# Kernel tuning notes

Measured on AMD Instinct MI355X. Metric: run time of the kernel, lower is better.

The kernel has to match this reference:

```python
import jax, jax.numpy as jnp
import numpy as np
import math

B, S, D, H = 2, 2048, 2048, 16
HD = D // H            # 128
FF = 4 * D             # 8192
EPS = 1e-5


def _alibi_slopes(num_heads):
    # power-of-2 path (16 heads): slopes = base^i, base = 2^(-2^-(log2(n)-3))
    closest = 2 ** math.floor(math.log2(num_heads))
    base = 2.0 ** (-(2.0 ** (-(math.log2(closest) - 3))))
    powers = np.arange(1, 1 + closest, dtype=np.float32)
    slopes = base ** powers
    if closest != num_heads:
        extra_base = 2.0 ** (-(2.0 ** (-(math.log2(2 * closest) - 3))))
        num_rem = min(closest, num_heads - closest)
        extra_powers = np.arange(1, 1 + 2 * num_rem, 2, dtype=np.float32)
        slopes = np.concatenate([slopes, extra_base ** extra_powers])
    return jnp.asarray(slopes, dtype=jnp.float32)


def setup_inputs() -> dict:
    key = jax.random.key(0)
    ks = jax.random.split(key, 8)
    s = 0.02
    return {
        "x": jax.random.normal(ks[0], (B, S, D), dtype=jnp.float32),
        "ln1_w": jnp.ones((D,), jnp.float32),
        "ln1_b": jnp.zeros((D,), jnp.float32),
        "wqkv": jax.random.normal(ks[1], (D, 3 * D), jnp.float32) * s,
        "bqkv": jnp.zeros((3 * D,), jnp.float32),
        "wo": jax.random.normal(ks[2], (D, D), jnp.float32) * s,
        "bo": jnp.zeros((D,), jnp.float32),
        "ln2_w": jnp.ones((D,), jnp.float32),
        "ln2_b": jnp.zeros((D,), jnp.float32),
        "w1": jax.random.normal(ks[3], (D, FF), jnp.float32) * s,
        "b1": jnp.zeros((FF,), jnp.float32),
        "w2": jax.random.normal(ks[4], (FF, D), jnp.float32) * s,
        "b2": jnp.zeros((D,), jnp.float32),
    }


def _ln(x, w, b):
    mu = jnp.mean(x, axis=-1, keepdims=True)
    var = jnp.mean(jnp.square(x - mu), axis=-1, keepdims=True)
    return (x - mu) * jax.lax.rsqrt(var + EPS) * w + b


def reference(x, ln1_w, ln1_b, wqkv, bqkv, wo, bo, ln2_w, ln2_b, w1, b1, w2, b2):
    slopes = _alibi_slopes(H)                      # [H]
    # --- input layernorm + attention ---
    h = _ln(x, ln1_w, ln1_b)
    qkv = h @ wqkv + bqkv                          # [B,S,3D]
    q, k, v = jnp.split(qkv, 3, axis=-1)
    q = q.reshape(B, S, H, HD).transpose(0, 2, 1, 3)  # [B,H,S,HD]
    k = k.reshape(B, S, H, HD).transpose(0, 2, 1, 3)
    v = v.reshape(B, S, H, HD).transpose(0, 2, 1, 3)
    scores = jnp.einsum("bhqd,bhkd->bhqk", q, k) / math.sqrt(HD)
    pos = jnp.arange(S, dtype=jnp.float32)
    rel = pos[None, :] - pos[:, None]              # j - i
    alibi = slopes[:, None, None] * rel[None]      # [H,S,S]
    scores = scores.astype(jnp.float32) + alibi[None]
    causal = rel <= 0                              # j <= i
    scores = jnp.where(causal[None, None], scores, jnp.finfo(jnp.float32).min)
    probs = jax.nn.softmax(scores, axis=-1).astype(x.dtype)
    attn = jnp.einsum("bhqk,bhkd->bhqd", probs, v)  # [B,H,S,HD]
    attn = attn.transpose(0, 2, 1, 3).reshape(B, S, D)
    x = x + attn @ wo + bo
    # --- post-attn layernorm + GELU MLP ---
    h2 = _ln(x, ln2_w, ln2_b)
    m = jax.nn.gelu(h2 @ w1 + b1, approximate=True) @ w2 + b2
    return x + m
```

## Files before the change

### kernel.cpp

```cpp
#include <hip/hip_runtime.h>
#include <hip/hip_bf16.h>
#include <stdint.h>

#define BB 2
#define SS 2048
#define DD 2048
#define HH 16
#define HD 128
#define FFD 8192
#define TD (3*DD)

typedef unsigned short u16;
typedef __attribute__((ext_vector_type(8))) short s16x8;
typedef __attribute__((ext_vector_type(4))) float f32x4;

struct alignas(8) U16x4 { u16 a, b, c, d; };

__device__ __forceinline__ u16 f2b(float f) {
  union { float f; uint32_t u; } v; v.f = f;
  uint32_t r = (v.u + 0x7fffu + ((v.u >> 16) & 1u)) >> 16;
  return (u16)r;
}

__device__ __forceinline__ void async16(const void* g, void* l) {
  __builtin_amdgcn_global_load_lds((const __attribute__((address_space(1))) void*)g,
                                   (__attribute__((address_space(3))) void*)l,
                                   16, 0, 0);
}

__global__ __launch_bounds__(256) void wconv_t(const float* __restrict__ W,
                                               u16* __restrict__ Wt, int K, int N) {
  __shared__ float tile[64][65];
  int k0 = blockIdx.x * 64, n0 = blockIdx.y * 64;
  int c = threadIdx.x & 63, r0 = threadIdx.x >> 6;
#pragma unroll
  for (int i = 0; i < 16; ++i) {
    int r = i * 4 + r0;
    tile[r][c] = W[(size_t)(k0 + r) * N + n0 + c];
  }
  __syncthreads();
#pragma unroll
  for (int i = 0; i < 16; ++i) {
    int n = i * 4 + r0;
    Wt[(size_t)(n0 + n) * K + k0 + c] = f2b(tile[c][n]);
  }
}

__global__ __launch_bounds__(256) void ln_kernel(const float* __restrict__ X,
                                                 const float* __restrict__ g,
                                                 const float* __restrict__ be,
                                                 u16* __restrict__ O) {
  int row = blockIdx.x;
  const float* xr = X + (size_t)row * DD;
  int t = threadIdx.x;
  float4 v0 = ((const float4*)xr)[t];
  float4 v1 = ((const float4*)xr)[t + 256];
  float s = v0.x + v0.y + v0.z + v0.w + v1.x + v1.y + v1.z + v1.w;
  float q = v0.x*v0.x + v0.y*v0.y + v0.z*v0.z + v0.w*v0.w
          + v1.x*v1.x + v1.y*v1.y + v1.z*v1.z + v1.w*v1.w;
#pragma unroll
  for (int o = 32; o > 0; o >>= 1) { s += __shfl_down(s, o); q += __shfl_down(q, o); }
  __shared__ float red[8];
  if ((t & 63) == 0) { red[t >> 6] = s; red[4 + (t >> 6)] = q; }
  __syncthreads();
  float S = red[0] + red[1] + red[2] + red[3];
  float Q = red[4] + red[5] + red[6] + red[7];
  float mu = S * (1.0f / DD);
  float var = Q * (1.0f / DD) - mu * mu;
  float rs = rsqrtf(var + 1e-5f);
  float4 g0 = ((const float4*)g)[t],  g1 = ((const float4*)g)[t + 256];
  float4 b0 = ((const float4*)be)[t], b1 = ((const float4*)be)[t + 256];
  U16x4 o0, o1;
  o0.a = f2b((v0.x - mu) * rs * g0.x + b0.x);
  o0.b = f2b((v0.y - mu) * rs * g0.y + b0.y);
  o0.c = f2b((v0.z - mu) * rs * g0.z + b0.z);
  o0.d = f2b((v0.w - mu) * rs * g0.w + b0.w);
  o1.a = f2b((v1.x - mu) * rs * g1.x + b1.x);
  o1.b = f2b((v1.y - mu) * rs * g1.y + b1.y);
  o1.c = f2b((v1.z - mu) * rs * g1.z + b1.z);
  o1.d = f2b((v1.w - mu) * rs * g1.w + b1.w);
  *(U16x4*)(O + (size_t)row * DD + t * 4)         = o0;
  *(U16x4*)(O + (size_t)row * DD + (t + 256) * 4) = o1;
}

template <int MODE>
__global__ __launch_bounds__(512, 2) void gemm8(const u16* __restrict__ A,
                                                const u16* __restrict__ Bt,
                                                const float* __restrict__ bias,
                                                const float* __restrict__ res,
                                                void* __restrict__ Cout,
                                                int M, int N, int K) {
  __shared__ __align__(16) u16 As[2][2][256 * 32];
  __shared__ __align__(16) u16 Bs[2][2][128 * 32];

  int n0 = blockIdx.x * 128, m0 = blockIdx.y * 256;
  int tid = threadIdx.x;
  int lane = tid & 63, w = tid >> 6;
  int wn = w & 1, wm = w >> 1;
  int col = lane & 15, quad = lane >> 4;

  int r = tid >> 2, sl = tid & 3;
  int gks = (sl ^ ((r >> 1) & 3)) * 8;
  const u16* ag = A  + (size_t)(m0 + r) * K + gks;
  const u16* bg = Bt + (size_t)(n0 + r) * K + gks;

  int swz = (col >> 1) & 3;
  int aoff = (wm * 64) * 32 + col * 32 + ((quad ^ swz) * 8);
  int boff = (wn * 64) * 32 + col * 32 + ((quad ^ swz) * 8);

  f32x4 acc[4][4] = {};
  int ntiles = K >> 6;

#pragma unroll
  for (int kh = 0; kh < 2; ++kh) {
    async16(ag + kh * 32, &As[0][kh][tid * 8]);
    async16(ag + (size_t)128 * K + kh * 32, &As[0][kh][4096 + tid * 8]);
    async16(bg + kh * 32, &Bs[0][kh][tid * 8]);
  }
  asm volatile("s_waitcnt vmcnt(0)" ::: "memory");
  __builtin_amdgcn_s_barrier();

  for (int t = 0; t < ntiles; ++t) {
    int p = t & 1, pn = p ^ 1;
    const u16* agn = ag + (t + 1) * 64;
    const u16* bgn = bg + (t + 1) * 64;
    bool pf = (t + 1 < ntiles);
#pragma unroll
    for (int kh = 0; kh < 2; ++kh) {
      const u16* as_ = As[p][kh];
      const u16* bs_ = Bs[p][kh];
      s16x8 af[4], bf[4];
#pragma unroll
      for (int i = 0; i < 4; ++i)
        bf[i] = *(const s16x8*)&bs_[boff + i * 512];
#pragma unroll
      for (int i = 0; i < 4; ++i)
        af[i] = *(const s16x8*)&as_[aoff + i * 512];
      if (pf) {
        async16(agn + kh * 32, &As[pn][kh][tid * 8]);
        async16(agn + (size_t)128 * K + kh * 32, &As[pn][kh][4096 + tid * 8]);
        async16(bgn + kh * 32, &Bs[pn][kh][tid * 8]);
        asm volatile("s_waitcnt vmcnt(3)" ::: "memory");
      } else if (kh == 0) {
        asm volatile("s_waitcnt vmcnt(0)" ::: "memory");
      }
      __builtin_amdgcn_s_barrier();
      __builtin_amdgcn_s_setprio(1);
#pragma unroll
      for (int i = 0; i < 4; ++i)
#pragma unroll
        for (int j = 0; j < 4; ++j)
          acc[i][j] = __builtin_amdgcn_mfma_f32_16x16x32_bf16(
              af[i], bf[j], acc[i][j], 0, 0, 0);
      __builtin_amdgcn_s_setprio(0);
      __builtin_amdgcn_s_barrier();
    }
  }

#pragma unroll
  for (int mt = 0; mt < 4; ++mt) {
    int mg = m0 + wm * 64 + mt * 16 + quad * 4;
#pragma unroll
    for (int nt = 0; nt < 4; ++nt) {
      int ng = n0 + wn * 64 + nt * 16 + col;
      float bn = bias[ng];
#pragma unroll
      for (int rr = 0; rr < 4; ++rr) {
        float v = acc[mt][nt][rr] + bn;
        size_t idx = (size_t)(mg + rr) * N + ng;
        if (MODE == 1) {
          float u = 1.5957691216057308f * (v + 0.044715f * v * v * v);
          v = v / (1.0f + __expf(-u));
        }
        if (MODE == 2) {
          ((float*)Cout)[idx] = v + res[idx];
        } else {
          ((u16*)Cout)[idx] = f2b(v);
        }
      }
    }
  }
}

__global__ __launch_bounds__(256) void attn_kernel(const u16* __restrict__ qkv,
                                                   u16* __restrict__ out) {
  __shared__ __align__(16) u16 Ks[2][64 * 128];
  __shared__ __align__(16) u16 Vts[128 * 64];
  __shared__ __align__(16) u16 Ps[4][16 * 72];
  int bx = blockIdx.x, h = blockIdx.y, b = blockIdx.z;
  int tid = threadIdx.x, lane = tid & 63, w = tid >> 6;
  int col = lane & 15, quad = lane >> 4;
  const u16* base  = qkv + (size_t)b * SS * TD + (size_t)h * HD;
  const u16* kbase = base + DD;
  const u16* vbase = base + 2 * DD;
  float slope = exp2f(-0.5f * (float)(h + 1));
  const float scale = 0.088388347648318447f;
  int krow = tid >> 4;
  int ghb = (tid & 15) ^ (krow & 7);
  int vkey_loc = tid >> 4;
  int vhd0 = (tid & 15) * 8;
  int kxc = 8 * (tid & 7);

#pragma unroll 1
  for (int ph = 0; ph < 2; ++ph) {
    int qt = ph ? (31 - bx) : bx;
    int q0 = qt * 64;
    int ntile = qt + 1;
    int qr = q0 + w * 16 + col;
    s16x8 qf[4];
#pragma unroll
    for (int c = 0; c < 4; ++c)
      qf[c] = *(const s16x8*)(base + (size_t)qr * TD + c * 32 + quad * 8);
    float m_i[4] = {-1e30f, -1e30f, -1e30f, -1e30f};
    float l_i[4] = {0.f, 0.f, 0.f, 0.f};
    f32x4 oacc[8] = {};
#pragma unroll
    for (int s = 0; s < 4; ++s)
      async16(kbase + (size_t)(s * 16 + krow) * TD + ghb * 8,
              &Ks[0][s * 2048 + tid * 8]);
    s16x8 vreg[4];
#pragma unroll
    for (int s = 0; s < 4; ++s)
      vreg[s] = *(const s16x8*)(vbase + (size_t)(s * 16 + vkey_loc) * TD + vhd0);

    for (int t = 0; t < ntile; ++t) {
      int j0 = t * 64;
      __syncthreads();
      if (t + 1 < ntile) {
#pragma unroll
        for (int s = 0; s < 4; ++s)
          async16(kbase + (size_t)(j0 + 64 + s * 16 + krow) * TD + ghb * 8,
                  &Ks[(t + 1) & 1][s * 2048 + tid * 8]);
      }
#pragma unroll
      for (int s = 0; s < 4; ++s) {
        int key = s * 16 + vkey_loc;
#pragma unroll
        for (int j = 0; j < 8; ++j)
          Vts[(vhd0 + j) * 64 + (key ^ kxc)] = (u16)vreg[s][j];
      }
      if (t + 1 < ntile) {
#pragma unroll
        for (int s = 0; s < 4; ++s)
          vreg[s] = *(const s16x8*)(vbase + (size_t)(j0 + 64 + s * 16 + vkey_loc) * TD + vhd0);
      }
      const u16* kt_ = Ks[t & 1];
      f32x4 sc[4];
#pragma unroll
      for (int nt = 0; nt < 4; ++nt) {
        f32x4 s4 = {0.f, 0.f, 0.f, 0.f};
        int key = nt * 16 + col;
        int ksw = col & 7;
#pragma unroll
        for (int c = 0; c < 4; ++c) {
          s16x8 kf = *(const s16x8*)&kt_[key * 128 + (((c * 4 + quad) ^ ksw) * 8)];
          s4 = __builtin_amdgcn_mfma_f32_16x16x32_bf16(qf[c], kf, s4, 0, 0, 0);
        }
        sc[nt] = s4;
      }
      int rb = q0 + w * 16 + quad * 4;
      float p[4][4];
      float mt_[4] = {-1e30f, -1e30f, -1e30f, -1e30f};
#pragma unroll
      for (int nt = 0; nt < 4; ++nt) {
        int j = j0 + nt * 16 + col;
#pragma unroll
        for (int rr = 0; rr < 4; ++rr) {
          float v = sc[nt][rr] * scale + slope * (float)(j - (rb + rr));
          if (j > rb + rr) v = -1e30f;
          p[nt][rr] = v;
          mt_[rr] = fmaxf(mt_[rr], v);
        }
      }
#pragma unroll
      for (int o = 1; o < 16; o <<= 1)
#pragma unroll
        for (int rr = 0; rr < 4; ++rr) mt_[rr] = fmaxf(mt_[rr], __shfl_xor(mt_[rr], o));
      float alpha[4];
#pragma unroll
      for (int rr = 0; rr < 4; ++rr) {
        float mn = fmaxf(m_i[rr], mt_[rr]);
        alpha[rr] = __expf(m_i[rr] - mn);
        m_i[rr] = mn;
      }
      float ls[4] = {0.f, 0.f, 0.f, 0.f};
#pragma unroll
      for (int nt = 0; nt < 4; ++nt)
#pragma unroll
        for (int rr = 0; rr < 4; ++rr) {
          float e = __expf(p[nt][rr] - m_i[rr]);
          p[nt][rr] = e;
          ls[rr] += e;
        }
#pragma unroll
      for (int o = 1; o < 16; o <<= 1)
#pragma unroll
        for (int rr = 0; rr < 4; ++rr) ls[rr] += __shfl_xor(ls[rr], o);
#pragma unroll
      for (int rr = 0; rr < 4; ++rr) l_i[rr] = l_i[rr] * alpha[rr] + ls[rr];
#pragma unroll
      for (int ot = 0; ot < 8; ++ot)
#pragma unroll
        for (int rr = 0; rr < 4; ++rr) oacc[ot][rr] *= alpha[rr];
#pragma unroll
      for (int nt = 0; nt < 4; ++nt)
#pragma unroll
        for (int rr = 0; rr < 4; ++rr)
          Ps[w][(quad * 4 + rr) * 72 + nt * 16 + col] = f2b(p[nt][rr]);
      __syncthreads();
#pragma unroll
      for (int kt = 0; kt < 2; ++kt) {
        s16x8 pf = *(const s16x8*)&Ps[w][col * 72 + kt * 32 + quad * 8];
        int k8 = kt * 32 + quad * 8;
#pragma unroll
        for (int ot = 0; ot < 8; ++ot) {
          int hd = ot * 16 + col;
          int swz = 8 * ((hd >> 3) & 7);
          s16x8 vf = *(const s16x8*)&Vts[hd * 64 + (k8 ^ swz)];
          oacc[ot] = __builtin_amdgcn_mfma_f32_16x16x32_bf16(pf, vf, oacc[ot], 0, 0, 0);
        }
      }
    }
#pragma unroll
    for (int rr = 0; rr < 4; ++rr) l_i[rr] = 1.0f / l_i[rr];
    u16* ob = out + ((size_t)b * SS + q0 + w * 16 + quad * 4) * DD + h * HD;
#pragma unroll
    for (int ot = 0; ot < 8; ++ot)
#pragma unroll
      for (int rr = 0; rr < 4; ++rr)
        ob[(size_t)rr * DD + ot * 16 + col] = f2b(oacc[ot][rr] * l_i[rr]);
  }
}

extern "C" void kernel_launch(void* const* d_in, const int* in_sizes, int n_in,
                              void* d_out, int out_size, void* d_ws, size_t ws_size,
                              hipStream_t stream) {
  const float* x    = (const float*)d_in[0];
  const float* ln1w = (const float*)d_in[1];
  const float* ln1b = (const float*)d_in[2];
  const float* wqkv = (const float*)d_in[3];
  const float* bqkv = (const float*)d_in[4];
  const float* wo   = (const float*)d_in[5];
  const float* bo   = (const float*)d_in[6];
  const float* ln2w = (const float*)d_in[7];
  const float* ln2b = (const float*)d_in[8];
  const float* w1   = (const float*)d_in[9];
  const float* b1   = (const float*)d_in[10];
  const float* w2   = (const float*)d_in[11];
  const float* b2   = (const float*)d_in[12];

  const int M = BB * SS;
  char* ws = (char*)d_ws;
  u16*  wt   = (u16*)ws;
  u16*  qkv  = (u16*)(ws + 33554432ull);
  u16*  cbuf = (u16*)(ws + 33554432ull + 50331648ull);
  float* r1  = (float*)(ws + 33554432ull + 50331648ull + 67108864ull);
  u16* h1 = cbuf;
  u16* attn = cbuf;
  u16* m1 = cbuf;
  u16* h2 = qkv;

  ln_kernel<<<M, 256, 0, stream>>>(x, ln1w, ln1b, h1);
  wconv_t<<<dim3(DD / 64, TD / 64), 256, 0, stream>>>(wqkv, wt, DD, TD);
  gemm8<0><<<dim3(TD / 128, M / 256), 512, 0, stream>>>(h1, wt, bqkv, nullptr, qkv, M, TD, DD);
  attn_kernel<<<dim3(16, HH, BB), 256, 0, stream>>>(qkv, attn);
  wconv_t<<<dim3(DD / 64, DD / 64), 256, 0, stream>>>(wo, wt, DD, DD);
  gemm8<2><<<dim3(DD / 128, M / 256), 512, 0, stream>>>(attn, wt, bo, x, r1, M, DD, DD);
  ln_kernel<<<M, 256, 0, stream>>>(r1, ln2w, ln2b, h2);
  wconv_t<<<dim3(DD / 64, FFD / 64), 256, 0, stream>>>(w1, wt, DD, FFD);
  gemm8<1><<<dim3(FFD / 128, M / 256), 512, 0, stream>>>(h2, wt, b1, nullptr, m1, M, FFD, DD);
  wconv_t<<<dim3(FFD / 64, DD / 64), 256, 0, stream>>>(w2, wt, FFD, DD);
  gemm8<2><<<dim3(DD / 128, M / 256), 512, 0, stream>>>(m1, wt, b2, r1, (float*)d_out, M, DD, FFD);
}
```

Measured before the change: 912.5 us.

## Add 256x256-tile bf16 GEMM kernel for QKV and FFN-up projections

Adds a new GEMM kernel with 256x256 output tiles, a 64-wide K step split into two 32-wide LDS halves, double-buffered async global-to-LDS loads interleaved with MFMA work, and raised wave priority around the MFMA blocks. It replaces the 256x128 tile kernel for the QKV and W1 projections, the two widest-N GEMMs. The aim is to raise arithmetic intensity and cut global and LDS traffic per FLOP. The grids become smaller: 24x16 blocks for QKV and 32x16 for W1. The kernel uses 128 KB of LDS and 128 accumulator floats per thread, which can limit occupancy and wave fill.

```diff
diff --git a/kernel.cpp b/kernel.cpp
--- a/kernel.cpp
+++ b/kernel.cpp
@@ -182,6 +182,114 @@
   }
 }
 
+template <int MODE>
+__global__ __launch_bounds__(512, 2) void gemm256(const u16* __restrict__ A,
+                                                  const u16* __restrict__ Bt,
+                                                  const float* __restrict__ bias,
+                                                  const float* __restrict__ res,
+                                                  void* __restrict__ Cout,
+                                                  int M, int N, int K) {
+  __shared__ __align__(16) u16 As[2][2][256 * 32];
+  __shared__ __align__(16) u16 Bs[2][2][256 * 32];
+
+  int n0 = blockIdx.x * 256, m0 = blockIdx.y * 256;
+  int tid = threadIdx.x;
+  int lane = tid & 63, w = tid >> 6;
+  int wn = w & 3, wm = w >> 2;
+  int col = lane & 15, quad = lane >> 4;
+
+  int r = tid >> 2, sl = tid & 3;
+  int gks = (sl ^ ((r >> 1) & 3)) * 8;
+  const u16* ag = A  + (size_t)(m0 + r) * K + gks;
+  const u16* bg = Bt + (size_t)(n0 + r) * K + gks;
+
+  int swz = (col >> 1) & 3;
+  int aoff = (wm * 128 + col) * 32 + ((quad ^ swz) * 8);
+  int boff = (wn * 64 + col) * 32 + ((quad ^ swz) * 8);
+
+  f32x4 acc[8][4] = {};
+  int ntiles = K >> 6;
+
+#pragma unroll
+  for (int kh = 0; kh < 2; ++kh) {
+    async16(ag + kh * 32, &As[0][kh][tid * 8]);
+    async16(ag + (size_t)128 * K + kh * 32, &As[0][kh][4096 + tid * 8]);
+    async16(bg + kh * 32, &Bs[0][kh][tid * 8]);
+    async16(bg + (size_t)128 * K + kh * 32, &Bs[0][kh][4096 + tid * 8]);
+  }
+  asm volatile("s_waitcnt vmcnt(0)" ::: "memory");
+  __builtin_amdgcn_s_barrier();
+
+  for (int t = 0; t < ntiles; ++t) {
+    int p = t & 1, pn = p ^ 1;
+    const u16* agn = ag + (t + 1) * 64;
+    const u16* bgn = bg + (t + 1) * 64;
+    bool pf = (t + 1 < ntiles);
+#pragma unroll
+    for (int kh = 0; kh < 2; ++kh) {
+      const u16* as_ = As[p][kh];
+      const u16* bs_ = Bs[p][kh];
+      s16x8 bf[4];
+#pragma unroll
+      for (int j = 0; j < 4; ++j)
+        bf[j] = *(const s16x8*)&bs_[boff + j * 512];
+#pragma unroll
+      for (int q = 0; q < 2; ++q) {
+        s16x8 af[4];
+#pragma unroll
+        for (int i = 0; i < 4; ++i)
+          af[i] = *(const s16x8*)&as_[aoff + q * 2048 + i * 512];
+        if (pf) {
+          if (q == 0) {
+            async16(agn + kh * 32, &As[pn][kh][tid * 8]);
+            async16(agn + (size_t)128 * K + kh * 32, &As[pn][kh][4096 + tid * 8]);
+          } else {
+            async16(bgn + kh * 32, &Bs[pn][kh][tid * 8]);
+            async16(bgn + (size_t)128 * K + kh * 32, &Bs[pn][kh][4096 + tid * 8]);
+            asm volatile("s_waitcnt vmcnt(4)" ::: "memory");
+          }
+        } else if (kh == 0 && q == 1) {
+          asm volatile("s_waitcnt vmcnt(0)" ::: "memory");
+        }
+        __builtin_amdgcn_s_barrier();
+        __builtin_amdgcn_s_setprio(1);
+#pragma unroll
+        for (int i = 0; i < 4; ++i)
+#pragma unroll
+          for (int j = 0; j < 4; ++j)
+            acc[q * 4 + i][j] = __builtin_amdgcn_mfma_f32_16x16x32_bf16(
+                af[i], bf[j], acc[q * 4 + i][j], 0, 0, 0);
+        __builtin_amdgcn_s_setprio(0);
+        __builtin_amdgcn_s_barrier();
+      }
+    }
+  }
+
+#pragma unroll
+  for (int mt = 0; mt < 8; ++mt) {
+    int mg = m0 + wm * 128 + mt * 16 + quad * 4;
+#pragma unroll
+    for (int nt = 0; nt < 4; ++nt) {
+      int ng = n0 + wn * 64 + nt * 16 + col;
+      float bn = bias[ng];
+#pragma unroll
+      for (int rr = 0; rr < 4; ++rr) {
+        float v = acc[mt][nt][rr] + bn;
+        size_t idx = (size_t)(mg + rr) * N + ng;
+        if (MODE == 1) {
+          float u = 1.5957691216057308f * (v + 0.044715f * v * v * v);
+          v = v / (1.0f + __expf(-u));
+        }
+        if (MODE == 2) {
+          ((float*)Cout)[idx] = v + res[idx];
+        } else {
+          ((u16*)Cout)[idx] = f2b(v);
+        }
+      }
+    }
+  }
+}
+
 __global__ __launch_bounds__(256) void attn_kernel(const u16* __restrict__ qkv,
                                                    u16* __restrict__ out) {
   __shared__ __align__(16) u16 Ks[2][64 * 128];
@@ -362,13 +470,13 @@
 
   ln_kernel<<<M, 256, 0, stream>>>(x, ln1w, ln1b, h1);
   wconv_t<<<dim3(DD / 64, TD / 64), 256, 0, stream>>>(wqkv, wt, DD, TD);
-  gemm8<0><<<dim3(TD / 128, M / 256), 512, 0, stream>>>(h1, wt, bqkv, nullptr, qkv, M, TD, DD);
+  gemm256<0><<<dim3(TD / 256, M / 256), 512, 0, stream>>>(h1, wt, bqkv, nullptr, qkv, M, TD, DD);
   attn_kernel<<<dim3(16, HH, BB), 256, 0, stream>>>(qkv, attn);
   wconv_t<<<dim3(DD / 64, DD / 64), 256, 0, stream>>>(wo, wt, DD, DD);
   gemm8<2><<<dim3(DD / 128, M / 256), 512, 0, stream>>>(attn, wt, bo, x, r1, M, DD, DD);
   ln_kernel<<<M, 256, 0, stream>>>(r1, ln2w, ln2b, h2);
   wconv_t<<<dim3(DD / 64, FFD / 64), 256, 0, stream>>>(w1, wt, DD, FFD);
-  gemm8<1><<<dim3(FFD / 128, M / 256), 512, 0, stream>>>(h2, wt, b1, nullptr, m1, M, FFD, DD);
+  gemm256<1><<<dim3(FFD / 256, M / 256), 512, 0, stream>>>(h2, wt, b1, nullptr, m1, M, FFD, DD);
   wconv_t<<<dim3(FFD / 64, DD / 64), 256, 0, stream>>>(w2, wt, FFD, DD);
   gemm8<2><<<dim3(DD / 128, M / 256), 512, 0, stream>>>(m1, wt, b2, r1, (float*)d_out, M, DD, FFD);
 }
```

Result: faster. 854.6 us (-6.3%).
